# Kernel tuning notes

Hardware: AMD Instinct MI355X
Metric: run time of the kernel (lower is better)

Reference implementation:

```python
import jax, jax.numpy as jnp
import numpy as np

NEG_SLOPE = 0.2
CLAMP = 1e9

C, N, T, IN_F = 8, 1024, 3, 64
H, OUT_F = 4, 64
E = 65536


def setup_inputs() -> dict:
    key = jax.random.key(0)
    k1, k2, k3, k4, k5 = jax.random.split(key, 5)
    edge_idx = jax.random.randint(k1, (2, E), 0, C * N, dtype=jnp.int64)
    node_feats = jax.random.normal(k2, (C, N, T, IN_F), dtype=jnp.float32)
    # xavier-ish scaling for parameters
    fc = jax.random.normal(k3, (T, IN_F, OUT_F * H), dtype=jnp.float32) * (2.0 / (IN_F + OUT_F * H)) ** 0.5
    attn_src = jax.random.normal(k4, (1, H, OUT_F * T), dtype=jnp.float32) * 0.1
    attn_dst = jax.random.normal(k5, (1, H, OUT_F * T), dtype=jnp.float32) * 0.1
    return {"edge_idx": edge_idx, "node_feats": node_feats, "fc": fc,
            "attn_src": attn_src, "attn_dst": attn_dst}


def reference(edge_idx, node_feats, fc, attn_src, attn_dst):
    c, n, t, f_in = node_feats.shape
    h = attn_src.shape[1]
    f_out = fc.shape[2] // h
    cn = c * n

    # per-node-type linear transform: (cn, t, in) x (t, in, h*out) -> (cn, t, h*out)
    hs = node_feats.reshape(cn, t, f_in)
    feat = jnp.einsum('bji,jik->bjk', hs, fc)

    # replicate the torch permute/reshape sequence exactly (row-major reshapes)
    x = feat.reshape(c, n, t, f_out * h)
    x = jnp.transpose(x, (0, 2, 1, 3))                  # (c, t, n, h*out)
    x = x.reshape(c, n, t, h, f_out)                    # torch .reshape on permuted copy
    x = jnp.transpose(x, (0, 1, 3, 2, 4))               # (c, n, h, t, out)
    feat_flat = x.reshape(cn, h, t * f_out)             # feat_src = feat_dst

    # node masks from edge endpoints (scatter 1s on rows)
    msrc = jnp.zeros((cn,), node_feats.dtype).at[edge_idx[0]].set(1.0)
    mdst = jnp.zeros((cn,), node_feats.dtype).at[edge_idx[1]].set(1.0)
    feat_src = feat_flat * msrc[:, None, None]
    feat_dst = feat_flat * mdst[:, None, None]

    a_src = jnp.clip(feat_src * attn_src, -CLAMP, CLAMP).reshape(c, n, h, f_out * t).sum(-1)
    a_dst = jnp.clip(feat_dst * attn_dst, -CLAMP, CLAMP).reshape(c, n, h, f_out * t).sum(-1)

    a = a_src[:, :, None, :] + a_dst[:, None, :, :]     # (c, n, n, h)
    a = jnp.where(a >= 0, a, NEG_SLOPE * a)             # leaky relu
    a = jnp.clip(a, -CLAMP, CLAMP)
    a = jax.nn.softmax(a, axis=0)                       # softmax over conformers (dim=0, as in source)

    fd = feat_dst.reshape(c, n, h, t * f_out)
    m = jnp.einsum('cvuh,cuhf->cvhf', a, fd)            # (c, n, h, t*out)
    m = jax.nn.relu(m)
    outs = m.reshape(c, n, h, t, f_out).sum(axis=2)     # (c, n, t, out)
    return outs, a
```

## Files before the change

kernel.cpp:

```cpp
#include <hip/hip_runtime.h>
#include <stdint.h>

#define CC 8
#define NN 1024
#define CN 8192
#define NE 65536
#define NEG_SLOPE 0.2f

typedef __attribute__((ext_vector_type(8))) short bf16x8;
typedef __attribute__((ext_vector_type(4))) float f32x4;

__device__ __forceinline__ ushort f2bfu(float x) {
    unsigned u = __float_as_uint(x);
    unsigned r = u + 0x7fffu + ((u >> 16) & 1u);
    return (ushort)(r >> 16);
}

__global__ void __launch_bounds__(256) k_feat(const float* __restrict__ nf,
                                              const float* __restrict__ fc,
                                              const int* __restrict__ edges,
                                              float* __restrict__ msrc, float* __restrict__ mdst,
                                              float* __restrict__ feat) {
    __shared__ float sFC[64][132];
    __shared__ float sHT[64][36];
    int t = threadIdx.x;
    int tt = blockIdx.y;
    if (tt == 0) {
        int e = blockIdx.x * 256 + t;
        if (e < NE) msrc[edges[e]] = 1.0f;
        else        mdst[edges[e]] = 1.0f;
    }
    int kh = blockIdx.x & 1;
    int r0 = (blockIdx.x >> 1) * 32;
    {
        const float* fcp = fc + tt * 16384 + kh * 128;
        #pragma unroll
        for (int i = 0; i < 8; ++i) {
            int f4 = t + 256 * i;
            int row = f4 >> 5, c4 = f4 & 31;
            *(float4*)&sFC[row][c4 * 4] = *(const float4*)(fcp + row * 256 + c4 * 4);
        }
    }
    {
        #pragma unroll
        for (int i = 0; i < 2; ++i) {
            int f4 = t + 256 * i;
            int r = f4 >> 4, c4 = f4 & 15;
            float4 v = *(const float4*)(nf + (size_t)(r0 + r) * 192 + tt * 64 + c4 * 4);
            sHT[c4 * 4 + 0][r] = v.x;
            sHT[c4 * 4 + 1][r] = v.y;
            sHT[c4 * 4 + 2][r] = v.z;
            sHT[c4 * 4 + 3][r] = v.w;
        }
    }
    __syncthreads();
    int rg = t >> 5;
    int kg = t & 31;
    float acc[4][4];
    #pragma unroll
    for (int a = 0; a < 4; ++a)
        #pragma unroll
        for (int b = 0; b < 4; ++b) acc[a][b] = 0.f;
    #pragma unroll 4
    for (int i = 0; i < 64; ++i) {
        float4 hv = *(const float4*)&sHT[i][rg * 4];
        float4 fv = *(const float4*)&sFC[i][kg * 4];
        const float* fp = (const float*)&fv;
        #pragma unroll
        for (int b = 0; b < 4; ++b) {
            acc[0][b] += hv.x * fp[b];
            acc[1][b] += hv.y * fp[b];
            acc[2][b] += hv.z * fp[b];
            acc[3][b] += hv.w * fp[b];
        }
    }
    #pragma unroll
    for (int a = 0; a < 4; ++a) {
        int b = r0 + rg * 4 + a;
        int c = b >> 10, n = b & 1023;
        float4 vv = {acc[a][0], acc[a][1], acc[a][2], acc[a][3]};
        *(float4*)(feat + (size_t)c * 786432 + (size_t)tt * 262144 + n * 256 + kh * 128 + kg * 4) = vv;
    }
}

__global__ void __launch_bounds__(256) k_rt(const float* __restrict__ feat,
                        const float* __restrict__ attn_src, const float* __restrict__ attn_dst,
                        const float* __restrict__ msrc, const float* __restrict__ mdst,
                        ushort* __restrict__ fdt, float* __restrict__ a_src, float* __restrict__ a_dst) {
    __shared__ ushort T[22560];
    int u0 = blockIdx.x * 64;
    int t2 = blockIdx.y;
    int c  = blockIdx.z;
    int t = threadIdx.x;
    int nl = t >> 2, q = t & 3;
    int b = (c << 10) + u0 + nl;
    float md = mdst[b], ms = msrc[b];
    const float* fp  = feat + (size_t)c * 786432 + (size_t)(u0 + nl) * 768 + t2 * 256 + q * 64;
    const float* wsp = attn_src + q * 192 + t2 * 64;
    const float* wdp = attn_dst + q * 192 + t2 * 64;
    float ssum = 0.f, dsum = 0.f;
    #pragma unroll
    for (int i4 = 0; i4 < 16; ++i4) {
        float4 v = *(const float4*)(fp + i4 * 4);
        const float* vv = (const float*)&v;
        #pragma unroll
        for (int k = 0; k < 4; ++k) {
            int f = i4 * 4 + k;
            ssum += vv[k] * wsp[f];
            dsum += vv[k] * wdp[f];
            T[(q * 64 + f) * 88 + q * 16 + nl] = f2bfu(vv[k] * md);
        }
    }
    atomicAdd(&a_src[(b << 2) + q], ssum * ms);
    atomicAdd(&a_dst[(b << 2) + q], dsum * md);
    __syncthreads();
    int h2 = t >> 6, j = t & 63;
    const ushort* row = &T[(h2 * 64 + j) * 88 + h2 * 16];
    ushort* dst = fdt + (size_t)((c * 4 + h2) * 192 + t2 * 64 + j) * 1024 + u0;
    #pragma unroll
    for (int i = 0; i < 8; ++i)
        *(uint4*)(dst + i * 8) = *(const uint4*)(row + i * 8);
}

__global__ void __launch_bounds__(256) k_att(const float* __restrict__ a_src,
                                             const float* __restrict__ a_dst,
                                             float* __restrict__ a_out, ushort* __restrict__ Abuf) {
    __shared__ float sAS[32];
    __shared__ ushort T2[32 * 520];
    int v = blockIdx.x;
    int t = threadIdx.x;
    if (t < 32) sAS[t] = a_src[((t >> 2) * 1024 + v) * 4 + (t & 3)];
    __syncthreads();
    int u0 = blockIdx.y * 512 + t;
    int u1 = u0 + 256;

    float mx0[4], mx1[4];
    #pragma unroll
    for (int h = 0; h < 4; ++h) { mx0[h] = -1e30f; mx1[h] = -1e30f; }
    #pragma unroll
    for (int c = 0; c < 8; ++c) {
        float4 d0 = *(const float4*)(a_dst + ((c << 10) + u0) * 4);
        float4 d1 = *(const float4*)(a_dst + ((c << 10) + u1) * 4);
        const float* dp0 = (const float*)&d0;
        const float* dp1 = (const float*)&d1;
        #pragma unroll
        for (int h = 0; h < 4; ++h) {
            float as = sAS[c * 4 + h];
            mx0[h] = fmaxf(mx0[h], as + dp0[h]);
            mx1[h] = fmaxf(mx1[h], as + dp1[h]);
        }
    }
    #pragma unroll
    for (int h = 0; h < 4; ++h) {
        float x = mx0[h];
        x = (x >= 0.f) ? x : NEG_SLOPE * x;
        mx0[h] = fminf(fmaxf(x, -1e9f), 1e9f);
        float y = mx1[h];
        y = (y >= 0.f) ? y : NEG_SLOPE * y;
        mx1[h] = fminf(fmaxf(y, -1e9f), 1e9f);
    }

    float s0[4] = {0.f, 0.f, 0.f, 0.f}, s1[4] = {0.f, 0.f, 0.f, 0.f};
    #pragma unroll
    for (int c = 0; c < 8; ++c) {
        float4 d0 = *(const float4*)(a_dst + ((c << 10) + u0) * 4);
        float4 d1 = *(const float4*)(a_dst + ((c << 10) + u1) * 4);
        const float* dp0 = (const float*)&d0;
        const float* dp1 = (const float*)&d1;
        #pragma unroll
        for (int h = 0; h < 4; ++h) {
            float as = sAS[c * 4 + h];
            float x = as + dp0[h];
            x = (x >= 0.f) ? x : NEG_SLOPE * x;
            x = fminf(fmaxf(x, -1e9f), 1e9f);
            s0[h] += __expf(x - mx0[h]);
            float y = as + dp1[h];
            y = (y >= 0.f) ? y : NEG_SLOPE * y;
            y = fminf(fmaxf(y, -1e9f), 1e9f);
            s1[h] += __expf(y - mx1[h]);
        }
    }
    float r0[4], r1[4];
    #pragma unroll
    for (int h = 0; h < 4; ++h) { r0[h] = 1.f / s0[h]; r1[h] = 1.f / s1[h]; }

    #pragma unroll
    for (int c = 0; c < 8; ++c) {
        float4 d0 = *(const float4*)(a_dst + ((c << 10) + u0) * 4);
        float4 d1 = *(const float4*)(a_dst + ((c << 10) + u1) * 4);
        const float* dp0 = (const float*)&d0;
        const float* dp1 = (const float*)&d1;
        float w0[4], w1[4];
        #pragma unroll
        for (int h = 0; h < 4; ++h) {
            float as = sAS[c * 4 + h];
            float x = as + dp0[h];
            x = (x >= 0.f) ? x : NEG_SLOPE * x;
            x = fminf(fmaxf(x, -1e9f), 1e9f);
            w0[h] = __expf(x - mx0[h]) * r0[h];
            float y = as + dp1[h];
            y = (y >= 0.f) ? y : NEG_SLOPE * y;
            y = fminf(fmaxf(y, -1e9f), 1e9f);
            w1[h] = __expf(y - mx1[h]) * r1[h];
        }
        float* ao0 = a_out + ((size_t)((c << 10) + v) * 1024 + u0) * 4;
        float* ao1 = a_out + ((size_t)((c << 10) + v) * 1024 + u1) * 4;
        *(float4*)ao0 = *(const float4*)w0;
        *(float4*)ao1 = *(const float4*)w1;
        #pragma unroll
        for (int h = 0; h < 4; ++h) {
            T2[(c * 4 + h) * 520 + t]       = f2bfu(w0[h]);
            T2[(c * 4 + h) * 520 + t + 256] = f2bfu(w1[h]);
        }
    }
    __syncthreads();
    #pragma unroll
    for (int i = 0; i < 8; ++i) {
        int id = t + 256 * i;
        int row = id >> 6;
        int c16 = id & 63;
        uint4 vv = *(const uint4*)&T2[row * 520 + c16 * 8];
        *(uint4*)(Abuf + (size_t)(row * 1024 + v) * 1024 + blockIdx.y * 512 + c16 * 8) = vv;
    }
}

__global__ void __launch_bounds__(512) k_gemm(const ushort* __restrict__ A,
                                              const ushort* __restrict__ B,
                                              float* __restrict__ Mout) {
    __shared__ ushort sA[128 * 72];
    __shared__ ushort sB[192 * 72];
    int ch = blockIdx.y;
    int v0 = blockIdx.x * 128;
    int t = threadIdx.x;
    const ushort* pA = A + (size_t)ch * (1024 * 1024) + (size_t)v0 * 1024;
    const ushort* pB = B + (size_t)ch * (192 * 1024);
    int wid = t >> 6, lane = t & 63;
    int wm = (wid >> 2) * 64, wn = (wid & 3) * 48;
    int lm = lane & 15, lq = lane >> 4;
    f32x4 acc[4][3];
    #pragma unroll
    for (int i = 0; i < 4; ++i)
        #pragma unroll
        for (int j = 0; j < 3; ++j)
            acc[i][j] = (f32x4){0.f, 0.f, 0.f, 0.f};
    for (int kk = 0; kk < 1024; kk += 64) {
        #pragma unroll
        for (int i = 0; i < 2; ++i) {
            int cid = t + 512 * i;
            int r = cid >> 3, kc = cid & 7;
            uint4 vv = *(const uint4*)(pA + (size_t)r * 1024 + kk + kc * 8);
            *(uint4*)&sA[r * 72 + kc * 8] = vv;
        }
        #pragma unroll
        for (int i = 0; i < 3; ++i) {
            int cid = t + 512 * i;
            int r = cid >> 3, kc = cid & 7;
            uint4 vv = *(const uint4*)(pB + (size_t)r * 1024 + kk + kc * 8);
            *(uint4*)&sB[r * 72 + kc * 8] = vv;
        }
        __syncthreads();
        #pragma unroll
        for (int ks = 0; ks < 64; ks += 32) {
            bf16x8 af[4], bg[3];
            #pragma unroll
            for (int i = 0; i < 4; ++i)
                af[i] = *(const bf16x8*)&sA[(wm + i * 16 + lm) * 72 + ks + lq * 8];
            #pragma unroll
            for (int j = 0; j < 3; ++j)
                bg[j] = *(const bf16x8*)&sB[(wn + j * 16 + lm) * 72 + ks + lq * 8];
            #pragma unroll
            for (int i = 0; i < 4; ++i)
                #pragma unroll
                for (int j = 0; j < 3; ++j)
                    acc[i][j] = __builtin_amdgcn_mfma_f32_16x16x32_bf16(af[i], bg[j], acc[i][j], 0, 0, 0);
        }
        __syncthreads();
    }
    float* pM = Mout + (size_t)ch * 196608 + (size_t)v0 * 192;
    #pragma unroll
    for (int i = 0; i < 4; ++i)
        #pragma unroll
        for (int r = 0; r < 4; ++r) {
            int row = wm + i * 16 + lq * 4 + r;
            #pragma unroll
            for (int j = 0; j < 3; ++j)
                pM[(size_t)row * 192 + wn + j * 16 + lm] = acc[i][j][r];
        }
}

__global__ void k_out(const float* __restrict__ Mm, float* __restrict__ outp) {
    int b = blockIdx.x;
    int c = b >> 10, v = b & 1023;
    int tf = threadIdx.x;
    float s = 0.f;
    #pragma unroll
    for (int h = 0; h < 4; ++h) {
        float x = Mm[(size_t)(c * 4 + h) * 196608 + (size_t)v * 192 + tf];
        s += fmaxf(x, 0.f);
    }
    outp[(size_t)b * 192 + tf] = s;
}

extern "C" void kernel_launch(void* const* d_in, const int* in_sizes, int n_in,
                              void* d_out, int out_size, void* d_ws, size_t ws_size,
                              hipStream_t stream) {
    const int*   edges  = (const int*)d_in[0];
    const float* nf     = (const float*)d_in[1];
    const float* fc     = (const float*)d_in[2];
    const float* asrc_w = (const float*)d_in[3];
    const float* adst_w = (const float*)d_in[4];
    float* outp  = (float*)d_out;
    float* a_out = outp + 1572864;

    char* ws = (char*)d_ws;
    float*  msrc  = (float*)(ws + 0);
    float*  mdst  = (float*)(ws + 32768);
    float*  a_src = (float*)(ws + 65536);
    float*  a_dst = (float*)(ws + 196608);
    ushort* fdt   = (ushort*)(ws + 327680);
    float*  feat  = (float*)(ws + 12910592);
    float*  Mm    = feat;
    ushort* Abuf  = (ushort*)(ws + 38076416);

    hipMemsetAsync(msrc, 0, 327680, stream);
    k_feat<<<dim3(512, 3), dim3(256), 0, stream>>>(nf, fc, edges, msrc, mdst, feat);
    k_rt<<<dim3(16, 3, 8), dim3(256), 0, stream>>>(feat, asrc_w, adst_w, msrc, mdst, fdt, a_src, a_dst);
    k_att<<<dim3(1024, 2), dim3(256), 0, stream>>>(a_src, a_dst, a_out, Abuf);
    k_gemm<<<dim3(8, 32), dim3(512), 0, stream>>>(Abuf, fdt, Mm);
    k_out<<<dim3(8192), dim3(192), 0, stream>>>(Mm, outp);
}
```

Measured before the change: 249.9 us.

## Drop bf16 attention buffer; GEMM reads fp32 attention output directly

The attention kernel no longer writes a transposed bf16 copy of the softmax weights. The GEMM now loads its A operand straight from the fp32 a_out tensor, using strided scalar loads, and converts to bf16 while staging into shared memory. This removes one 64MB write and the LDS transpose in k_att. In exchange the GEMM reads twice as many bytes for A, and its loads are strided (stride 16 bytes per element) rather than coalesced 16-byte vectors, which may waste bandwidth.

```diff
diff --git a/kernel.cpp b/kernel.cpp
--- a/kernel.cpp
+++ b/kernel.cpp
@@ -124,9 +124,8 @@
 
 __global__ void __launch_bounds__(256) k_att(const float* __restrict__ a_src,
                                              const float* __restrict__ a_dst,
-                                             float* __restrict__ a_out, ushort* __restrict__ Abuf) {
+                                             float* __restrict__ a_out) {
     __shared__ float sAS[32];
-    __shared__ ushort T2[32 * 520];
     int v = blockIdx.x;
     int t = threadIdx.x;
     if (t < 32) sAS[t] = a_src[((t >> 2) * 1024 + v) * 4 + (t & 3)];
@@ -207,24 +206,10 @@
         float* ao1 = a_out + ((size_t)((c << 10) + v) * 1024 + u1) * 4;
         *(float4*)ao0 = *(const float4*)w0;
         *(float4*)ao1 = *(const float4*)w1;
-        #pragma unroll
-        for (int h = 0; h < 4; ++h) {
-            T2[(c * 4 + h) * 520 + t]       = f2bfu(w0[h]);
-            T2[(c * 4 + h) * 520 + t + 256] = f2bfu(w1[h]);
-        }
-    }
-    __syncthreads();
-    #pragma unroll
-    for (int i = 0; i < 8; ++i) {
-        int id = t + 256 * i;
-        int row = id >> 6;
-        int c16 = id & 63;
-        uint4 vv = *(const uint4*)&T2[row * 520 + c16 * 8];
-        *(uint4*)(Abuf + (size_t)(row * 1024 + v) * 1024 + blockIdx.y * 512 + c16 * 8) = vv;
-    }
-}
-
-__global__ void __launch_bounds__(512) k_gemm(const ushort* __restrict__ A,
+    }
+}
+
+__global__ void __launch_bounds__(512) k_gemm(const float* __restrict__ Aout,
                                               const ushort* __restrict__ B,
                                               float* __restrict__ Mout) {
     __shared__ ushort sA[128 * 72];
@@ -232,7 +217,9 @@
     int ch = blockIdx.y;
     int v0 = blockIdx.x * 128;
     int t = threadIdx.x;
-    const ushort* pA = A + (size_t)ch * (1024 * 1024) + (size_t)v0 * 1024;
+    int c1024 = (ch >> 2) << 10;
+    int h = ch & 3;
+    const float* pAf = Aout + (size_t)(c1024 + v0) * 4096 + h;
     const ushort* pB = B + (size_t)ch * (192 * 1024);
     int wid = t >> 6, lane = t & 63;
     int wm = (wid >> 2) * 64, wn = (wid & 3) * 48;
@@ -245,11 +232,11 @@
             acc[i][j] = (f32x4){0.f, 0.f, 0.f, 0.f};
     for (int kk = 0; kk < 1024; kk += 64) {
         #pragma unroll
-        for (int i = 0; i < 2; ++i) {
-            int cid = t + 512 * i;
-            int r = cid >> 3, kc = cid & 7;
-            uint4 vv = *(const uint4*)(pA + (size_t)r * 1024 + kk + kc * 8);
-            *(uint4*)&sA[r * 72 + kc * 8] = vv;
+        for (int i = 0; i < 16; ++i) {
+            int id = t + 512 * i;
+            int r = id >> 6, u = id & 63;
+            float p = pAf[(size_t)r * 4096 + (kk + u) * 4];
+            sA[r * 72 + u] = f2bfu(p);
         }
         #pragma unroll
         for (int i = 0; i < 3; ++i) {
@@ -320,12 +307,11 @@
     ushort* fdt   = (ushort*)(ws + 327680);
     float*  feat  = (float*)(ws + 12910592);
     float*  Mm    = feat;
-    ushort* Abuf  = (ushort*)(ws + 38076416);
 
     hipMemsetAsync(msrc, 0, 327680, stream);
     k_feat<<<dim3(512, 3), dim3(256), 0, stream>>>(nf, fc, edges, msrc, mdst, feat);
     k_rt<<<dim3(16, 3, 8), dim3(256), 0, stream>>>(feat, asrc_w, adst_w, msrc, mdst, fdt, a_src, a_dst);
-    k_att<<<dim3(1024, 2), dim3(256), 0, stream>>>(a_src, a_dst, a_out, Abuf);
-    k_gemm<<<dim3(8, 32), dim3(512), 0, stream>>>(Abuf, fdt, Mm);
+    k_att<<<dim3(1024, 2), dim3(256), 0, stream>>>(a_src, a_dst, a_out);
+    k_gemm<<<dim3(8, 32), dim3(512), 0, stream>>>(a_out, fdt, Mm);
     k_out<<<dim3(8192), dim3(192), 0, stream>>>(Mm, outp);
 }
```

After: 258.0 us. 1.03x slower.
